# Kernel optimization log

Measured on AMD Instinct MI355X. Metric: run time of the kernel, lower is better.

Reference implementation:

```python
import jax, jax.numpy as jnp
import numpy as np

B, S, D, H = 2, 2048, 1024, 16
HD = D // H


def setup_inputs() -> dict:
    key = jax.random.key(0)
    ks = jax.random.split(key, 7)
    scale = 1.0 / np.sqrt(D)
    x = jax.random.normal(ks[0], (B, S, D), dtype=jnp.float32)
    att_mask = jax.random.randint(ks[1], (B, S, S), 0, 2, dtype=jnp.int32)
    Wq = jax.random.normal(ks[2], (D, D), dtype=jnp.float32) * scale
    Wk = jax.random.normal(ks[3], (D, D), dtype=jnp.float32) * scale
    Wv = jax.random.normal(ks[4], (D, D), dtype=jnp.float32) * scale
    Wo = jax.random.normal(ks[5], (D, D), dtype=jnp.float32) * scale
    bo = jnp.zeros((D,), dtype=jnp.float32)
    return {"x": x, "att_mask": att_mask, "Wq": Wq, "Wk": Wk, "Wv": Wv, "Wo": Wo, "bo": bo}


def reference(x, att_mask, Wq, Wk, Wv, Wo, bo):
    # Self-attention: kv_source = x, kv_len = q_len = S
    b, s, d = x.shape
    # projections; weights stored as (d_in, d_out)
    q = (x @ Wq).reshape(b, s, H, HD).transpose(0, 2, 1, 3)  # (B,H,S,HD)
    k = (x @ Wk).reshape(b, s, H, HD).transpose(0, 2, 1, 3)
    v = (x @ Wv).reshape(b, s, H, HD).transpose(0, 2, 1, 3)

    scores = jnp.einsum("bhqd,bhkd->bhqk", q, k) / jnp.sqrt(jnp.float32(HD))
    mask = att_mask.astype(bool)[:, None, :, :]  # (B,1,S,S)
    scores = jnp.where(mask, scores, -jnp.inf)

    # Recover fully-masked rows: set their first column score to 0.0
    all_masked = jnp.all(jnp.isneginf(scores), axis=-1, keepdims=True)  # (B,H,S,1)
    first_col = jnp.arange(s) == 0  # (S,)
    scores = jnp.where(all_masked & first_col, 0.0, scores)

    weights = jax.nn.softmax(scores, axis=-1)  # dropout is identity in eval mode
    ctx = jnp.einsum("bhqk,bhkd->bhqd", weights, v)  # (B,H,S,HD)
    ctx = ctx.transpose(0, 2, 1, 3).reshape(b, s, d)
    return ctx @ Wo + bo
```

## Files before the change

kernel.cpp:

```cpp
#include <hip/hip_runtime.h>
#include <stdint.h>

typedef unsigned short u16;
typedef unsigned int u32;
typedef __attribute__((ext_vector_type(8))) short bf16x8;
typedef __attribute__((ext_vector_type(4))) float f32x4;
typedef __attribute__((ext_vector_type(4))) u32 u32x4;

#define MFMA16(a, b, c) __builtin_amdgcn_mfma_f32_16x16x32_bf16((a), (b), (c), 0, 0, 0)

#define QSCALE 0.18033688011112042f

#define BIT_SMEAR(x, r) ((u32)(((int)((x) << (31 - (r)))) >> 31))

__device__ __forceinline__ u16 f2bf(float f) {
  u32 u = __float_as_uint(f);
  u += 0x7fffu + ((u >> 16) & 1u);
  return (u16)(u >> 16);
}

__device__ __forceinline__ u32 cvt_pk_bf16(float a, float b) {
  u32 r;
  asm("v_cvt_pk_bf16_f32 %0, %1, %2" : "=v"(r) : "v"(a), "v"(b));
  return r;
}

__device__ __forceinline__ void load_lds16(const void* g, void* l) {
  __builtin_amdgcn_global_load_lds((const __attribute__((address_space(1))) void*)g,
                                   (__attribute__((address_space(3))) void*)l, 16, 0, 0);
}

__device__ __forceinline__ int swz8(int row, int cb) {
  return row * 128 + ((cb ^ (row & 7)) << 4);
}

__global__ __launch_bounds__(256) void prep_kernel(const float4* __restrict__ x,
                                                   const int* __restrict__ mask,
                                                   const float* __restrict__ W0,
                                                   const float* __restrict__ W1,
                                                   const float* __restrict__ W2,
                                                   const float* __restrict__ W3,
                                                   ushort4* __restrict__ xbf,
                                                   u16* __restrict__ wt,
                                                   u32* __restrict__ MB) {
  const int bid = blockIdx.x, tid = threadIdx.x;
  __shared__ float t[32][33];
  __shared__ u32 nib[4][64];
  if (bid < 1024) {
    for (int i = bid * 256 + tid; i < 1048576; i += 262144) {
      float4 v = x[i];
      ushort4 o;
      o.x = f2bf(v.x); o.y = f2bf(v.y); o.z = f2bf(v.z); o.w = f2bf(v.w);
      xbf[i] = o;
    }
  } else if (bid < 5120) {
    int r = bid - 1024;
    const int z = r >> 10; r &= 1023;
    const int by = (r >> 5) << 5, bx = (r & 31) << 5;
    const float* W = (z == 0) ? W0 : (z == 1) ? W1 : (z == 2) ? W2 : W3;
    u16* o = wt + (size_t)z * 1048576;
    const int tx = tid & 31, ty = tid >> 5;
#pragma unroll
    for (int j = 0; j < 32; j += 8) t[ty + j][tx] = W[(size_t)(by + ty + j) * 1024 + bx + tx];
    __syncthreads();
#pragma unroll
    for (int j = 0; j < 32; j += 8) o[(size_t)(bx + ty + j) * 1024 + by + tx] = f2bf(t[tx][ty + j]);
  } else {
    const int wave = tid >> 6, lane = tid & 63;
    const int gw = (bid - 5120) * 4 + wave;
    for (int r = gw; r < 32768; r += 4096) {
      const int row = r >> 3, kb = (r & 7) << 8;
      int4 v = *(const int4*)(mask + (size_t)row * 2048 + kb + lane * 4);
      nib[wave][lane] = (v.x ? 1u : 0u) | (v.y ? 2u : 0u) | (v.z ? 4u : 0u) | (v.w ? 8u : 0u);
      if (lane < 8) {
        const u32* p = &nib[wave][lane << 3];
        u32 a = p[0] | (p[1] << 4) | (p[2] << 8) | (p[3] << 12) |
                (p[4] << 16) | (p[5] << 20) | (p[6] << 24) | (p[7] << 28);
        MB[(size_t)row * 64 + (kb >> 5) + lane] = a;
      }
    }
  }
}

template <int MODE>
__global__ __launch_bounds__(256) void gemm_kernel(const u16* __restrict__ A,
                                                   const u16* __restrict__ Bt,
                                                   u16* __restrict__ Qo, u16* __restrict__ Ko,
                                                   u16* __restrict__ Vo, float* __restrict__ Fo,
                                                   const float* __restrict__ bias) {
  __shared__ u16 As[64 * 64];
  __shared__ u16 Bs[128 * 64];
  const int tid = threadIdx.x, lane = tid & 63;
  const int l15 = lane & 15, g = lane >> 4;
  const int wave = tid >> 6, wr = wave >> 1, wc = wave & 1;
  const int bid = blockIdx.x;
  const int xcd = bid & 7, bi = bid >> 3;
  int m0, n0;
  if (MODE == 0) {
    m0 = (((xcd & 3) << 4) + (bi & 15)) * 64;
    n0 = ((xcd >> 2) * 12 + (bi >> 4)) * 128;
  } else {
    m0 = ((xcd << 3) + (bi & 7)) * 64;
    n0 = (bi >> 3) * 128;
  }
  const int xo = (((tid & 7) ^ ((tid >> 3) & 7)) << 4);
  const char* Ag = (const char*)A + (size_t)(m0 + (tid >> 3)) * 2048 + xo;
  const char* Bg = (const char*)Bt + (size_t)(n0 + (tid >> 3)) * 2048 + xo;
  char* Asc = (char*)As;
  char* Bsc = (char*)Bs;
  char* ldA = Asc + wave * 1024;
  char* ldB = Bsc + wave * 1024;

  f32x4 acc[2][4] = {};

  for (int kt = 0; kt < 16; ++kt) {
    const int kbyte = kt * 128;
    __syncthreads();
    load_lds16(Ag + kbyte, ldA);
    load_lds16(Ag + kbyte + 32 * 2048, ldA + 4096);
#pragma unroll
    for (int p = 0; p < 4; ++p)
      load_lds16(Bg + kbyte + p * 65536, ldB + p * 4096);
    __syncthreads();

    bf16x8 af[2][2], bfr[4][2];
#pragma unroll
    for (int i = 0; i < 2; ++i) {
      const int ra = wr * 32 + i * 16 + l15;
      af[i][0] = *(const bf16x8*)(Asc + swz8(ra, g));
      af[i][1] = *(const bf16x8*)(Asc + swz8(ra, 4 + g));
    }
#pragma unroll
    for (int j = 0; j < 4; ++j) {
      const int rb = wc * 64 + j * 16 + l15;
      bfr[j][0] = *(const bf16x8*)(Bsc + swz8(rb, g));
      bfr[j][1] = *(const bf16x8*)(Bsc + swz8(rb, 4 + g));
    }
#pragma unroll
    for (int kk = 0; kk < 2; ++kk)
#pragma unroll
      for (int i = 0; i < 2; ++i)
#pragma unroll
        for (int j = 0; j < 4; ++j)
          acc[i][j] = MFMA16(af[i][kk], bfr[j][kk], acc[i][j]);
  }

  if (MODE == 1) {
#pragma unroll
    for (int i = 0; i < 2; ++i) {
      const int mrow = m0 + wr * 32 + i * 16 + g * 4;
#pragma unroll
      for (int j = 0; j < 4; ++j) {
        const int col = n0 + wc * 64 + j * 16 + l15;
        f32x4 v = acc[i][j];
#pragma unroll
        for (int r = 0; r < 4; ++r)
          Fo[(size_t)(mrow + r) * 1024 + col] = v[r] + bias[col];
      }
    }
  } else {
    const int which = n0 >> 10;
    const float scale = (which == 0) ? QSCALE : 1.0f;
    u16* outp = (which == 0) ? Qo : (which == 1) ? Ko : Vo;
#pragma unroll
    for (int i = 0; i < 2; ++i) {
      const int mrow = m0 + wr * 32 + i * 16 + g * 4;
      const int bb = mrow >> 11, s = mrow & 2047;
#pragma unroll
      for (int j = 0; j < 4; ++j) {
        const int col = (n0 + wc * 64 + j * 16 + l15) & 1023;
        const int h = col >> 6, hd = col & 63;
        f32x4 v = acc[i][j];
        if (which == 2) {
          const int qb = (s >> 2) & 15;
          const int half = (qb >> 2) & 1;
          const int chunk = (qb & 3) | ((qb & 8) >> 1);
          const int sp = (s & ~63) | (chunk << 3) | (half << 2);
          u32 w0 = cvt_pk_bf16(v[0], v[1]);
          u32 w1 = cvt_pk_bf16(v[2], v[3]);
          *(uint2*)(outp + ((((size_t)(bb * 16 + h)) * 64 + hd) * 2048 + sp)) = make_uint2(w0, w1);
        } else {
#pragma unroll
          for (int r = 0; r < 4; ++r)
            outp[(((size_t)(bb * 16 + h)) * 2048 + s + r) * 64 + hd] = f2bf(v[r] * scale);
        }
      }
    }
  }
}

__global__ __launch_bounds__(256, 2) void attn_kernel(const u16* __restrict__ Q,
                                                      const u16* __restrict__ K,
                                                      const u16* __restrict__ VT,
                                                      const u32* __restrict__ MB,
                                                      u16* __restrict__ CTX) {
  __shared__ u16 Kl[2][8192];
  __shared__ u16 Vl[2][8192];
  const int tid = threadIdx.x, lane = tid & 63, wave = tid >> 6;
  const int l15 = lane & 15, g = lane >> 4;
  const int L = blockIdx.x + (blockIdx.y << 4);
  const int bh = ((L & 7) << 2) + ((L >> 3) & 3);
  const int q0 = (L >> 5) * 128;
  const int b = bh >> 4, h = bh & 15;
  const int qw0 = q0 + wave * 32;

  const char* Qb = (const char*)Q + ((size_t)bh * 2048 + qw0) * 128;
  const bf16x8 aq00 = *(const bf16x8*)(Qb + l15 * 128 + g * 16);
  const bf16x8 aq01 = *(const bf16x8*)(Qb + l15 * 128 + 64 + g * 16);
  const bf16x8 aq10 = *(const bf16x8*)(Qb + (16 + l15) * 128 + g * 16);
  const bf16x8 aq11 = *(const bf16x8*)(Qb + (16 + l15) * 128 + 64 + g * 16);

  const char* Kg = (const char*)K + (size_t)bh * 2048 * 128;
  const char* Vg = (const char*)VT + (size_t)bh * 64 * 4096;
  const u32* mp0 = MB + ((size_t)b * 2048 + qw0 + l15) * 64;
  const u32* mp1 = mp0 + 16 * 64;

  const int lane8 = lane >> 3;
  const int xo = ((lane & 7) ^ lane8) << 4;
  const char* KsrcL = Kg + (size_t)lane8 * 128 + xo;
  const char* VsrcL = Vg + (size_t)lane8 * 4096 + xo;
  const int vhd = (wave & 1) * 32;
  const int vsub = wave >> 1;

  int koff[4][2], voff[2][4];
#pragma unroll
  for (int i = 0; i < 4; ++i) {
    koff[i][0] = swz8(i * 16 + l15, g);
    koff[i][1] = swz8(i * 16 + l15, 4 + g);
  }
#pragma unroll
  for (int ks = 0; ks < 2; ++ks)
#pragma unroll
    for (int j = 0; j < 4; ++j) voff[ks][j] = swz8(j * 16 + l15, ks * 4 + g);

  f32x4 oacc[4][2] = {};
  float lrow[2] = {0.f, 0.f};

  {
    char* Kd = (char*)Kl[0] + wave * 4096;
    char* Vd = (char*)Vl[0] + wave * 4096;
#pragma unroll
    for (int p = 0; p < 4; ++p) {
      load_lds16(KsrcL + wave * 4096 + p * 1024, Kd + p * 1024);
      load_lds16(VsrcL + (size_t)(vhd + p * 8) * 4096 + vsub * 128, Vd + p * 1024);
    }
  }
  uint4 mcA = *(const uint4*)mp0;
  uint4 mcB = *(const uint4*)mp1;
  __syncthreads();

  int cur = 0;
  for (int kb = 0; kb < 16; ++kb) {
    const int kn = (kb < 15) ? kb + 1 : 15;
    if (kb < 15) {
      char* Kd = (cur ? (char*)Kl[0] : (char*)Kl[1]) + wave * 4096;
      char* Vd = (cur ? (char*)Vl[0] : (char*)Vl[1]) + wave * 4096;
#pragma unroll
      for (int p = 0; p < 4; ++p) {
        load_lds16(KsrcL + (size_t)kn * 16384 + wave * 4096 + p * 1024, Kd + p * 1024);
        load_lds16(VsrcL + (size_t)(vhd + p * 8) * 4096 + (size_t)(2 * kn + vsub) * 128,
                   Vd + p * 1024);
      }
    }
    uint4 mnA = *(const uint4*)(mp0 + (size_t)kn * 4);
    uint4 mnB = *(const uint4*)(mp1 + (size_t)kn * 4);

#pragma unroll
    for (int s = 0; s < 2; ++s) {
      const char* Kc = (const char*)Kl[cur] + s * 8192;
      const char* Vc = (const char*)Vl[cur] + s * 8192;
      const u32 mA0 = s ? mcA.z : mcA.x, mA1 = s ? mcA.w : mcA.y;
      const u32 mB0 = s ? mcB.z : mcB.x, mB1 = s ? mcB.w : mcB.y;

      f32x4 sa[2][4];
      __builtin_amdgcn_s_setprio(1);
#pragma unroll
      for (int i = 0; i < 4; ++i) {
        const int sh = (i & 1) * 16 + g * 4;
        const u32 invA = ~(((i & 2) ? mA1 : mA0) >> sh);
        const u32 invB = ~(((i & 2) ? mB1 : mB0) >> sh);
        f32x4 bA, bB;
#pragma unroll
        for (int r = 0; r < 4; ++r) {
          bA[r] = __int_as_float(BIT_SMEAR(invA, r) & 0xFF7F0000u);
          bB[r] = __int_as_float(BIT_SMEAR(invB, r) & 0xFF7F0000u);
        }
        bf16x8 bk0 = *(const bf16x8*)(Kc + koff[i][0]);
        bf16x8 bk1 = *(const bf16x8*)(Kc + koff[i][1]);
        sa[0][i] = MFMA16(bk1, aq01, MFMA16(bk0, aq00, bA));
        sa[1][i] = MFMA16(bk1, aq11, MFMA16(bk0, aq10, bB));
      }
      __builtin_amdgcn_s_setprio(0);

      u32 Wp[2][8];
#pragma unroll
      for (int f = 0; f < 2; ++f) {
        float ps = 0.f;
#pragma unroll
        for (int i = 0; i < 4; ++i) {
          const float p0 = __builtin_amdgcn_exp2f(sa[f][i][0]);
          const float p1 = __builtin_amdgcn_exp2f(sa[f][i][1]);
          const float p2 = __builtin_amdgcn_exp2f(sa[f][i][2]);
          const float p3 = __builtin_amdgcn_exp2f(sa[f][i][3]);
          ps += (p0 + p1) + (p2 + p3);
          Wp[f][i * 2] = cvt_pk_bf16(p0, p1);
          Wp[f][i * 2 + 1] = cvt_pk_bf16(p2, p3);
        }
        lrow[f] += ps;
      }

      __builtin_amdgcn_s_setprio(1);
#pragma unroll
      for (int ks = 0; ks < 2; ++ks) {
        u32x4 t0 = {Wp[0][ks * 4], Wp[0][ks * 4 + 1], Wp[0][ks * 4 + 2], Wp[0][ks * 4 + 3]};
        u32x4 t1 = {Wp[1][ks * 4], Wp[1][ks * 4 + 1], Wp[1][ks * 4 + 2], Wp[1][ks * 4 + 3]};
        const bf16x8 ap0 = __builtin_bit_cast(bf16x8, t0);
        const bf16x8 ap1 = __builtin_bit_cast(bf16x8, t1);
#pragma unroll
        for (int j = 0; j < 4; ++j) {
          bf16x8 bv = *(const bf16x8*)(Vc + voff[ks][j]);
          oacc[j][0] = MFMA16(bv, ap0, oacc[j][0]);
          oacc[j][1] = MFMA16(bv, ap1, oacc[j][1]);
        }
      }
      __builtin_amdgcn_s_setprio(0);
      __builtin_amdgcn_sched_barrier(0);
    }

    __syncthreads();
    cur ^= 1;
    mcA = mnA;
    mcB = mnB;
  }

#pragma unroll
  for (int f = 0; f < 2; ++f) {
    float lr = lrow[f];
    lr += __shfl_xor(lr, 16);
    lr += __shfl_xor(lr, 32);
    const float inv = 1.0f / fmaxf(lr, 1e-30f);
    u16* Cb = CTX + ((size_t)(b * 2048 + qw0 + f * 16 + l15)) * 1024 + h * 64 + g * 4;
#pragma unroll
    for (int j = 0; j < 4; ++j) {
      u32 w0 = cvt_pk_bf16(oacc[j][f][0] * inv, oacc[j][f][1] * inv);
      u32 w1 = cvt_pk_bf16(oacc[j][f][2] * inv, oacc[j][f][3] * inv);
      *(uint2*)(Cb + j * 16) = make_uint2(w0, w1);
    }
  }
}

extern "C" void kernel_launch(void* const* d_in, const int* in_sizes, int n_in,
                              void* d_out, int out_size, void* d_ws, size_t ws_size,
                              hipStream_t stream) {
  const float* x   = (const float*)d_in[0];
  const int* amask = (const int*)d_in[1];
  const float* Wq  = (const float*)d_in[2];
  const float* Wk  = (const float*)d_in[3];
  const float* Wv  = (const float*)d_in[4];
  const float* Wo  = (const float*)d_in[5];
  const float* bo  = (const float*)d_in[6];

  char* ws = (char*)d_ws;
  u16* xbf  = (u16*)(ws);
  u16* wt   = (u16*)(ws + 8388608);
  u16* Qb   = (u16*)(ws + 16777216);
  u16* Kb   = (u16*)(ws + 25165824);
  u16* VT   = (u16*)(ws + 33554432);
  u16* CTX  = (u16*)(ws + 41943040);
  u32* MB   = (u32*)(ws + 50331648);

  prep_kernel<<<6144, 256, 0, stream>>>((const float4*)x, amask, Wq, Wk, Wv, Wo,
                                        (ushort4*)xbf, wt, MB);

  gemm_kernel<0><<<1536, 256, 0, stream>>>(xbf, wt, Qb, Kb, VT, nullptr, nullptr);

  attn_kernel<<<dim3(16, 32), 256, 0, stream>>>(Qb, Kb, VT, MB, CTX);

  gemm_kernel<1><<<512, 256, 0, stream>>>(CTX, wt + 3145728, nullptr, nullptr, nullptr,
                                          (float*)d_out, bo);
}
```

Baseline: 121.3 us.

## Shrink attention tile to 64 queries and 64 keys, doubling block count

The attention kernel now processes 64 query rows per block (16 per wave instead of 32) and 64-key chunks per step (32 iterations instead of 16), with halved LDS buffers and launch bounds raised to 4 blocks per SM. The grid doubles to 1024 blocks. The goal is more parallelism and occupancy across the GPU's CUs. In exchange, each K/V tile loaded into LDS is reused by half as many queries, and each block does more synchronization steps.

```diff
diff --git a/kernel.cpp b/kernel.cpp
--- a/kernel.cpp
+++ b/kernel.cpp
@@ -189,38 +189,34 @@
   }
 }
 
-__global__ __launch_bounds__(256, 2) void attn_kernel(const u16* __restrict__ Q,
+__global__ __launch_bounds__(256, 4) void attn_kernel(const u16* __restrict__ Q,
                                                       const u16* __restrict__ K,
                                                       const u16* __restrict__ VT,
                                                       const u32* __restrict__ MB,
                                                       u16* __restrict__ CTX) {
-  __shared__ u16 Kl[2][8192];
-  __shared__ u16 Vl[2][8192];
+  __shared__ u16 Kl[2][4096];
+  __shared__ u16 Vl[2][4096];
   const int tid = threadIdx.x, lane = tid & 63, wave = tid >> 6;
   const int l15 = lane & 15, g = lane >> 4;
-  const int L = blockIdx.x + (blockIdx.y << 4);
+  const int L = blockIdx.x + (blockIdx.y << 5);
   const int bh = ((L & 7) << 2) + ((L >> 3) & 3);
-  const int q0 = (L >> 5) * 128;
+  const int q0 = (L >> 5) * 64;
   const int b = bh >> 4, h = bh & 15;
-  const int qw0 = q0 + wave * 32;
+  const int qw0 = q0 + wave * 16;
 
   const char* Qb = (const char*)Q + ((size_t)bh * 2048 + qw0) * 128;
-  const bf16x8 aq00 = *(const bf16x8*)(Qb + l15 * 128 + g * 16);
-  const bf16x8 aq01 = *(const bf16x8*)(Qb + l15 * 128 + 64 + g * 16);
-  const bf16x8 aq10 = *(const bf16x8*)(Qb + (16 + l15) * 128 + g * 16);
-  const bf16x8 aq11 = *(const bf16x8*)(Qb + (16 + l15) * 128 + 64 + g * 16);
+  const bf16x8 aq0 = *(const bf16x8*)(Qb + l15 * 128 + g * 16);
+  const bf16x8 aq1 = *(const bf16x8*)(Qb + l15 * 128 + 64 + g * 16);
 
   const char* Kg = (const char*)K + (size_t)bh * 2048 * 128;
   const char* Vg = (const char*)VT + (size_t)bh * 64 * 4096;
-  const u32* mp0 = MB + ((size_t)b * 2048 + qw0 + l15) * 64;
-  const u32* mp1 = mp0 + 16 * 64;
+  const u32* mp = MB + ((size_t)b * 2048 + qw0 + l15) * 64;
 
   const int lane8 = lane >> 3;
   const int xo = ((lane & 7) ^ lane8) << 4;
   const char* KsrcL = Kg + (size_t)lane8 * 128 + xo;
   const char* VsrcL = Vg + (size_t)lane8 * 4096 + xo;
-  const int vhd = (wave & 1) * 32;
-  const int vsub = wave >> 1;
+  const int wo = wave * 2048;
 
   int koff[4][2], voff[2][4];
 #pragma unroll
@@ -233,119 +229,94 @@
 #pragma unroll
     for (int j = 0; j < 4; ++j) voff[ks][j] = swz8(j * 16 + l15, ks * 4 + g);
 
-  f32x4 oacc[4][2] = {};
-  float lrow[2] = {0.f, 0.f};
-
-  {
-    char* Kd = (char*)Kl[0] + wave * 4096;
-    char* Vd = (char*)Vl[0] + wave * 4096;
-#pragma unroll
-    for (int p = 0; p < 4; ++p) {
-      load_lds16(KsrcL + wave * 4096 + p * 1024, Kd + p * 1024);
-      load_lds16(VsrcL + (size_t)(vhd + p * 8) * 4096 + vsub * 128, Vd + p * 1024);
-    }
-  }
-  uint4 mcA = *(const uint4*)mp0;
-  uint4 mcB = *(const uint4*)mp1;
+  f32x4 oacc[4] = {};
+  float lrow = 0.f;
+
+#pragma unroll
+  for (int p = 0; p < 2; ++p) {
+    load_lds16(KsrcL + wo + p * 1024, (char*)Kl[0] + wo + p * 1024);
+    load_lds16(VsrcL + (size_t)(wave * 16 + p * 8) * 4096, (char*)Vl[0] + wo + p * 1024);
+  }
+  uint2 mc = *(const uint2*)mp;
   __syncthreads();
 
   int cur = 0;
-  for (int kb = 0; kb < 16; ++kb) {
-    const int kn = (kb < 15) ? kb + 1 : 15;
-    if (kb < 15) {
-      char* Kd = (cur ? (char*)Kl[0] : (char*)Kl[1]) + wave * 4096;
-      char* Vd = (cur ? (char*)Vl[0] : (char*)Vl[1]) + wave * 4096;
-#pragma unroll
-      for (int p = 0; p < 4; ++p) {
-        load_lds16(KsrcL + (size_t)kn * 16384 + wave * 4096 + p * 1024, Kd + p * 1024);
-        load_lds16(VsrcL + (size_t)(vhd + p * 8) * 4096 + (size_t)(2 * kn + vsub) * 128,
+  for (int kb = 0; kb < 32; ++kb) {
+    const int kn = kb + 1;
+    if (kb < 31) {
+      char* Kd = (cur ? (char*)Kl[0] : (char*)Kl[1]) + wo;
+      char* Vd = (cur ? (char*)Vl[0] : (char*)Vl[1]) + wo;
+#pragma unroll
+      for (int p = 0; p < 2; ++p) {
+        load_lds16(KsrcL + (size_t)kn * 8192 + wo + p * 1024, Kd + p * 1024);
+        load_lds16(VsrcL + (size_t)(wave * 16 + p * 8) * 4096 + (size_t)kn * 128,
                    Vd + p * 1024);
       }
     }
-    uint4 mnA = *(const uint4*)(mp0 + (size_t)kn * 4);
-    uint4 mnB = *(const uint4*)(mp1 + (size_t)kn * 4);
-
-#pragma unroll
-    for (int s = 0; s < 2; ++s) {
-      const char* Kc = (const char*)Kl[cur] + s * 8192;
-      const char* Vc = (const char*)Vl[cur] + s * 8192;
-      const u32 mA0 = s ? mcA.z : mcA.x, mA1 = s ? mcA.w : mcA.y;
-      const u32 mB0 = s ? mcB.z : mcB.x, mB1 = s ? mcB.w : mcB.y;
-
-      f32x4 sa[2][4];
-      __builtin_amdgcn_s_setprio(1);
-#pragma unroll
-      for (int i = 0; i < 4; ++i) {
-        const int sh = (i & 1) * 16 + g * 4;
-        const u32 invA = ~(((i & 2) ? mA1 : mA0) >> sh);
-        const u32 invB = ~(((i & 2) ? mB1 : mB0) >> sh);
-        f32x4 bA, bB;
-#pragma unroll
-        for (int r = 0; r < 4; ++r) {
-          bA[r] = __int_as_float(BIT_SMEAR(invA, r) & 0xFF7F0000u);
-          bB[r] = __int_as_float(BIT_SMEAR(invB, r) & 0xFF7F0000u);
-        }
-        bf16x8 bk0 = *(const bf16x8*)(Kc + koff[i][0]);
-        bf16x8 bk1 = *(const bf16x8*)(Kc + koff[i][1]);
-        sa[0][i] = MFMA16(bk1, aq01, MFMA16(bk0, aq00, bA));
-        sa[1][i] = MFMA16(bk1, aq11, MFMA16(bk0, aq10, bB));
-      }
-      __builtin_amdgcn_s_setprio(0);
-
-      u32 Wp[2][8];
-#pragma unroll
-      for (int f = 0; f < 2; ++f) {
-        float ps = 0.f;
-#pragma unroll
-        for (int i = 0; i < 4; ++i) {
-          const float p0 = __builtin_amdgcn_exp2f(sa[f][i][0]);
-          const float p1 = __builtin_amdgcn_exp2f(sa[f][i][1]);
-          const float p2 = __builtin_amdgcn_exp2f(sa[f][i][2]);
-          const float p3 = __builtin_amdgcn_exp2f(sa[f][i][3]);
-          ps += (p0 + p1) + (p2 + p3);
-          Wp[f][i * 2] = cvt_pk_bf16(p0, p1);
-          Wp[f][i * 2 + 1] = cvt_pk_bf16(p2, p3);
-        }
-        lrow[f] += ps;
-      }
-
-      __builtin_amdgcn_s_setprio(1);
-#pragma unroll
-      for (int ks = 0; ks < 2; ++ks) {
-        u32x4 t0 = {Wp[0][ks * 4], Wp[0][ks * 4 + 1], Wp[0][ks * 4 + 2], Wp[0][ks * 4 + 3]};
-        u32x4 t1 = {Wp[1][ks * 4], Wp[1][ks * 4 + 1], Wp[1][ks * 4 + 2], Wp[1][ks * 4 + 3]};
-        const bf16x8 ap0 = __builtin_bit_cast(bf16x8, t0);
-        const bf16x8 ap1 = __builtin_bit_cast(bf16x8, t1);
-#pragma unroll
-        for (int j = 0; j < 4; ++j) {
-          bf16x8 bv = *(const bf16x8*)(Vc + voff[ks][j]);
-          oacc[j][0] = MFMA16(bv, ap0, oacc[j][0]);
-          oacc[j][1] = MFMA16(bv, ap1, oacc[j][1]);
-        }
-      }
-      __builtin_amdgcn_s_setprio(0);
-      __builtin_amdgcn_sched_barrier(0);
-    }
+    uint2 mn = *(const uint2*)(mp + ((kb < 31) ? (size_t)kn * 2 : (size_t)kb * 2));
+
+    const char* Kc = (const char*)Kl[cur];
+    const char* Vc = (const char*)Vl[cur];
+
+    f32x4 sa[4];
+    __builtin_amdgcn_s_setprio(1);
+#pragma unroll
+    for (int i = 0; i < 4; ++i) {
+      const int sh = (i & 1) * 16 + g * 4;
+      const u32 inv = ~(((i & 2) ? mc.y : mc.x) >> sh);
+      f32x4 bA;
+#pragma unroll
+      for (int r = 0; r < 4; ++r)
+        bA[r] = __int_as_float(BIT_SMEAR(inv, r) & 0xFF7F0000u);
+      bf16x8 bk0 = *(const bf16x8*)(Kc + koff[i][0]);
+      bf16x8 bk1 = *(const bf16x8*)(Kc + koff[i][1]);
+      sa[i] = MFMA16(bk1, aq1, MFMA16(bk0, aq0, bA));
+    }
+    __builtin_amdgcn_s_setprio(0);
+
+    u32 Wp[8];
+    float ps = 0.f;
+#pragma unroll
+    for (int i = 0; i < 4; ++i) {
+      const float p0 = __builtin_amdgcn_exp2f(sa[i][0]);
+      const float p1 = __builtin_amdgcn_exp2f(sa[i][1]);
+      const float p2 = __builtin_amdgcn_exp2f(sa[i][2]);
+      const float p3 = __builtin_amdgcn_exp2f(sa[i][3]);
+      ps += (p0 + p1) + (p2 + p3);
+      Wp[i * 2] = cvt_pk_bf16(p0, p1);
+      Wp[i * 2 + 1] = cvt_pk_bf16(p2, p3);
+    }
+    lrow += ps;
+
+    __builtin_amdgcn_s_setprio(1);
+#pragma unroll
+    for (int ks = 0; ks < 2; ++ks) {
+      u32x4 t0 = {Wp[ks * 4], Wp[ks * 4 + 1], Wp[ks * 4 + 2], Wp[ks * 4 + 3]};
+      const bf16x8 ap = __builtin_bit_cast(bf16x8, t0);
+#pragma unroll
+      for (int j = 0; j < 4; ++j) {
+        bf16x8 bv = *(const bf16x8*)(Vc + voff[ks][j]);
+        oacc[j] = MFMA16(bv, ap, oacc[j]);
+      }
+    }
+    __builtin_amdgcn_s_setprio(0);
+    __builtin_amdgcn_sched_barrier(0);
 
     __syncthreads();
     cur ^= 1;
-    mcA = mnA;
-    mcB = mnB;
-  }
-
-#pragma unroll
-  for (int f = 0; f < 2; ++f) {
-    float lr = lrow[f];
-    lr += __shfl_xor(lr, 16);
-    lr += __shfl_xor(lr, 32);
-    const float inv = 1.0f / fmaxf(lr, 1e-30f);
-    u16* Cb = CTX + ((size_t)(b * 2048 + qw0 + f * 16 + l15)) * 1024 + h * 64 + g * 4;
-#pragma unroll
-    for (int j = 0; j < 4; ++j) {
-      u32 w0 = cvt_pk_bf16(oacc[j][f][0] * inv, oacc[j][f][1] * inv);
-      u32 w1 = cvt_pk_bf16(oacc[j][f][2] * inv, oacc[j][f][3] * inv);
-      *(uint2*)(Cb + j * 16) = make_uint2(w0, w1);
-    }
+    mc = mn;
+  }
+
+  float lr = lrow;
+  lr += __shfl_xor(lr, 16);
+  lr += __shfl_xor(lr, 32);
+  const float inv = 1.0f / fmaxf(lr, 1e-30f);
+  u16* Cb = CTX + ((size_t)(b * 2048 + qw0 + l15)) * 1024 + h * 64 + g * 4;
+#pragma unroll
+  for (int j = 0; j < 4; ++j) {
+    u32 w0 = cvt_pk_bf16(oacc[j][0] * inv, oacc[j][1] * inv);
+    u32 w1 = cvt_pk_bf16(oacc[j][2] * inv, oacc[j][3] * inv);
+    *(uint2*)(Cb + j * 16) = make_uint2(w0, w1);
   }
 }
 
@@ -374,7 +345,7 @@
 
   gemm_kernel<0><<<1536, 256, 0, stream>>>(xbf, wt, Qb, Kb, VT, nullptr, nullptr);
 
-  attn_kernel<<<dim3(16, 32), 256, 0, stream>>>(Qb, Kb, VT, MB, CTX);
+  attn_kernel<<<dim3(32, 32), 256, 0, stream>>>(Qb, Kb, VT, MB, CTX);
 
   gemm_kernel<1><<<512, 256, 0, stream>>>(CTX, wt + 3145728, nullptr, nullptr, nullptr,
                                           (float*)d_out, bo);
```

Measured after the change: 124.6 us. +2.7%, slower.
